# Performance work log

Measured on AMD Instinct MI355X. Metric: run time of the kernel, lower is better.

Reference implementation:

```python
import jax, jax.numpy as jnp
import numpy as np

B, CIN, H, W = 16, 1024, 32, 32
WIDTH = 256          # bottleneck width = planes * base_width/64 * cardinality
OUT = 1024           # planes * expansion
HEADS = WIDTH // 8   # 32
KS = 3               # kernel_size of SelfAttLayer


def unfold3x3(x):
    # x: (B, C, H, W) -> (B, C, 9, H, W), torch.nn.Unfold(3, padding=1) ordering (row-major kernel)
    xp = jnp.pad(x, ((0, 0), (0, 0), (1, 1), (1, 1)))
    h, w = x.shape[2], x.shape[3]
    patches = [xp[:, :, i:i + h, j:j + w] for i in range(KS) for j in range(KS)]
    return jnp.stack(patches, axis=2)


def bn(x, s, b):
    # inference-mode BatchNorm2d with running stats folded into per-channel scale/bias
    return x * s[None, :, None, None] + b[None, :, None, None]


def conv1x1(x, w):
    # w: (Cout, Cin)
    return jnp.einsum('bchw,oc->bohw', x, w)


def setup_inputs() -> dict:
    key = jax.random.key(0)
    ks = jax.random.split(key, 16)
    f = lambda k, shp, scale: (jax.random.normal(k, shp, dtype=jnp.float32) * scale)
    inp = {
        'x': f(ks[0], (B, CIN, H, W), 1.0),
        'w_conv1': f(ks[1], (WIDTH, CIN), 1.0 / np.sqrt(CIN)),
        'bn1_s': jnp.ones((WIDTH,), jnp.float32), 'bn1_b': jnp.zeros((WIDTH,), jnp.float32),
        'wq': f(ks[2], (WIDTH, WIDTH), 1.0 / np.sqrt(WIDTH)),
        'bnq_s': jnp.ones((WIDTH,), jnp.float32), 'bnq_b': jnp.zeros((WIDTH,), jnp.float32),
        'wk': f(ks[3], (WIDTH, WIDTH), 1.0 / np.sqrt(WIDTH)),
        'bnk_s': jnp.ones((WIDTH,), jnp.float32), 'bnk_b': jnp.zeros((WIDTH,), jnp.float32),
        'wv': f(ks[4], (WIDTH, WIDTH), 1.0 / np.sqrt(WIDTH)),
        'bnv_s': jnp.ones((WIDTH,), jnp.float32), 'bnv_b': jnp.zeros((WIDTH,), jnp.float32),
        'pos_h': f(ks[5], (WIDTH, KS, 1), 1.0),
        'pos_w': f(ks[6], (WIDTH, 1, KS), 1.0),
        'bnatt_s': jnp.ones((WIDTH,), jnp.float32), 'bnatt_b': jnp.zeros((WIDTH,), jnp.float32),
        'w_conv3': f(ks[7], (OUT, WIDTH), 1.0 / np.sqrt(WIDTH)),
        'bn3_s': jnp.ones((OUT,), jnp.float32), 'bn3_b': jnp.zeros((OUT,), jnp.float32),
    }
    return inp


def self_att(x, wq, bnq_s, bnq_b, wk, bnk_s, bnk_b, wv, bnv_s, bnv_b,
             pos_h, pos_w, bnatt_s, bnatt_b):
    b, c, h, w = x.shape
    d = c // HEADS
    q = jax.nn.relu(bn(conv1x1(x, wq), bnq_s, bnq_b))          # (B,C,H,W)
    k = jax.nn.relu(bn(conv1x1(x, wk), bnk_s, bnk_b))          # key_ks=1 -> 1x1 conv
    v = bn(conv1x1(x, wv), bnv_s, bnv_b)
    unfold_k = unfold3x3(k)                                     # (B,C,9,H,W)
    pos = (pos_h + pos_w).reshape(1, c, KS * KS, 1, 1)          # (1,C,9,1,1)
    kp = (unfold_k + pos).reshape(b, HEADS, d, KS * KS, h, w)
    qh = q.reshape(b, HEADS, d, h, w)
    attn = jnp.einsum('bgdhw,bgdkhw->bgkhw', qh, kp)            # (B,heads,9,H,W)
    attn = jax.nn.softmax(attn, axis=2)
    # local conv: each channel-group of size d shares its head's attention weights
    v_unf = unfold3x3(v).reshape(b, HEADS, d, KS * KS, h, w)
    out = jnp.einsum('bgdkhw,bgkhw->bgdhw', v_unf, attn).reshape(b, c, h, w)
    return jax.nn.relu(bn(out, bnatt_s, bnatt_b))


def reference(x, w_conv1, bn1_s, bn1_b, wq, bnq_s, bnq_b, wk, bnk_s, bnk_b,
              wv, bnv_s, bnv_b, pos_h, pos_w, bnatt_s, bnatt_b,
              w_conv3, bn3_s, bn3_b):
    residual = x
    h = jax.nn.relu(bn(conv1x1(x, w_conv1), bn1_s, bn1_b))
    h = self_att(h, wq, bnq_s, bnq_b, wk, bnk_s, bnk_b, wv, bnv_s, bnv_b,
                 pos_h, pos_w, bnatt_s, bnatt_b)
    h = bn(conv1x1(h, w_conv3), bn3_s, bn3_b)
    return jax.nn.relu(h + residual)
```

## Files before the change

### kernel.cpp

```cpp
#include <hip/hip_runtime.h>
#include <stdint.h>


typedef __attribute__((ext_vector_type(4))) float f32x4;
typedef __attribute__((ext_vector_type(8))) __bf16 bf16x8;
typedef __attribute__((ext_vector_type(4))) unsigned short u16x4;
typedef __attribute__((ext_vector_type(8))) unsigned short u16x8;

__device__ __forceinline__ float bf2f(unsigned short u) {
  union { unsigned int i; float f; } c; c.i = ((unsigned int)u) << 16; return c.f;
}
__device__ __forceinline__ unsigned short f2bf(float f) {
  union { float f; unsigned int i; } c; c.f = f;
  unsigned int x = c.i;
  return (unsigned short)((x + 0x7FFFu + ((x >> 16) & 1u)) >> 16);
}
__device__ __forceinline__ void gload_lds16(const unsigned short* g, unsigned short* l) {
  __builtin_amdgcn_global_load_lds(
      (const __attribute__((address_space(1))) unsigned int*)(const void*)g,
      (__attribute__((address_space(3))) unsigned int*)(void*)l, 16, 0, 0);
}

__global__ __launch_bounds__(256) void k_prep(
    const float* __restrict__ x, unsigned short* __restrict__ xt,
    const float* __restrict__ w1, const float* __restrict__ wq,
    const float* __restrict__ wk, const float* __restrict__ wv,
    const float* __restrict__ w3,
    const float* __restrict__ sq, const float* __restrict__ sk,
    const float* __restrict__ sv, const float* __restrict__ bq,
    const float* __restrict__ bk, const float* __restrict__ bv,
    unsigned short* __restrict__ w1b, unsigned short* __restrict__ wqkvb,
    unsigned short* __restrict__ w3b, float* __restrict__ sqkv,
    float* __restrict__ bqkv) {
  const int bid = blockIdx.x;
  if (bid < 16384) {
    __shared__ float tile[32][33];
    const int p0 = (bid & 31) * 32;
    const int c0 = ((bid >> 5) & 31) * 32;
    const int b  = bid >> 10;
    const int tx = threadIdx.x & 31;
    const int ty = threadIdx.x >> 5;
    const float* xb = x + (size_t)b * 1048576;
    unsigned short* xtb = xt + (size_t)b * 1048576;
#pragma unroll
    for (int i = 0; i < 4; ++i)
      tile[ty + i * 8][tx] = xb[(size_t)(c0 + ty + i * 8) * 1024 + p0 + tx];
    __syncthreads();
#pragma unroll
    for (int i = 0; i < 4; ++i)
      xtb[(size_t)(p0 + ty + i * 8) * 1024 + c0 + tx] = f2bf(tile[tx][ty + i * 8]);
    return;
  }
  const int idx = (bid - 16384) * 256 + threadIdx.x;
  if (idx < 262144) { w1b[idx] = f2bf(w1[idx]); return; }
  if (idx < 327680) { wqkvb[idx - 262144] = f2bf(wq[idx - 262144]); return; }
  if (idx < 393216) { wqkvb[idx - 262144] = f2bf(wk[idx - 327680]); return; }
  if (idx < 458752) { wqkvb[idx - 262144] = f2bf(wv[idx - 393216]); return; }
  if (idx < 720896) { w3b[idx - 458752] = f2bf(w3[idx - 458752]); return; }
  if (idx < 721664) {
    const int i = idx - 720896;
    sqkv[i] = i < 256 ? sq[i] : (i < 512 ? sk[i - 256] : sv[i - 512]);
    return;
  }
  if (idx < 722432) {
    const int i = idx - 721664;
    bqkv[i] = i < 256 ? bq[i] : (i < 512 ? bk[i - 256] : bv[i - 512]);
  }
}

template <int MF, int NF, int MODE>
__global__ __launch_bounds__(256, 3) void k_gemm_bt(
    const unsigned short* __restrict__ A, const unsigned short* __restrict__ B,
    void* __restrict__ CoutV, const float* __restrict__ scale,
    const float* __restrict__ bias, const unsigned short* __restrict__ resid_bf,
    int K, int relu_mask) {
  constexpr int BM = MF * 32, BN = NF * 32;
  __shared__ unsigned short lA[2][BM * 32];
  __shared__ unsigned short lB[2][BN * 32];
  const int m0 = blockIdx.y * BM;
  const int n0 = blockIdx.x * BN;
  const int tid = threadIdx.x;
  const int lane = tid & 63, wid = tid >> 6;
  const int wm = (wid >> 1) * (MF * 16), wn = (wid & 1) * (NF * 16);
  const int fr = lane & 15, fq = lane >> 4;
  const int cgr = (fq ^ (fr & 3)) * 8;

  f32x4 acc[MF][NF] = {};

  const int sr  = lane >> 2;
  const int scg = ((lane & 3) ^ (sr & 3)) * 8;
  const int warA = wid * (MF * 8);
  const int warB = wid * (NF * 8);
  const unsigned short* Asrc = A + (size_t)(m0 + warA + sr) * K + scg;
  const unsigned short* Bsrc = B + (size_t)(n0 + warB + sr) * K + scg;

  float rres[MF][NF][4];
  if (MODE == 1) {
#pragma unroll
    for (int i = 0; i < MF; ++i) {
      const int og = m0 + wm + i * 16 + fq * 4;
#pragma unroll
      for (int j = 0; j < NF; ++j) {
        const int P = n0 + wn + j * 16 + fr;
        const u16x4 rv = *(const u16x4*)&resid_bf[(size_t)P * 1024 + og];
#pragma unroll
        for (int rr = 0; rr < 4; ++rr) rres[i][j][rr] = bf2f(rv[rr]);
      }
    }
  }

#pragma unroll
  for (int u = 0; u < MF / 2; ++u)
    gload_lds16(Asrc + (size_t)u * 16 * K, &lA[0][(warA + u * 16) * 32]);
#pragma unroll
  for (int u = 0; u < NF / 2; ++u)
    gload_lds16(Bsrc + (size_t)u * 16 * K, &lB[0][(warB + u * 16) * 32]);
  __syncthreads();

  int p = 0;
  for (int k0 = 0; k0 < K; k0 += 32) {
    if (k0 + 32 < K) {
#pragma unroll
      for (int u = 0; u < MF / 2; ++u)
        gload_lds16(Asrc + (size_t)u * 16 * K + k0 + 32, &lA[p ^ 1][(warA + u * 16) * 32]);
#pragma unroll
      for (int u = 0; u < NF / 2; ++u)
        gload_lds16(Bsrc + (size_t)u * 16 * K + k0 + 32, &lB[p ^ 1][(warB + u * 16) * 32]);
    }

    bf16x8 af[MF], bb[NF];
#pragma unroll
    for (int i = 0; i < MF; ++i)
      af[i] = *(const bf16x8*)&lA[p][(wm + i * 16 + fr) * 32 + cgr];
#pragma unroll
    for (int j = 0; j < NF; ++j)
      bb[j] = *(const bf16x8*)&lB[p][(wn + j * 16 + fr) * 32 + cgr];
#pragma unroll
    for (int i = 0; i < MF; ++i)
#pragma unroll
      for (int j = 0; j < NF; ++j)
        acc[i][j] = __builtin_amdgcn_mfma_f32_16x16x32_bf16(af[i], bb[j], acc[i][j], 0, 0, 0);

    __syncthreads();
    p ^= 1;
  }

#pragma unroll
  for (int i = 0; i < MF; ++i) {
    const int og = m0 + wm + i * 16 + fq * 4;
    const f32x4 s4 = *(const f32x4*)&scale[og];
    const f32x4 b4 = *(const f32x4*)&bias[og];
#pragma unroll
    for (int j = 0; j < NF; ++j) {
      const int P = n0 + wn + j * 16 + fr;
      if (MODE == 0) {
        unsigned short* Cout = (unsigned short*)CoutV;
        const int do_relu = (relu_mask >> (og >> 8)) & 1;
        const size_t obase = (size_t)(og >> 8) * 4194304 + (size_t)P * 256 + (og & 255);
        u16x4 pk;
#pragma unroll
        for (int rr = 0; rr < 4; ++rr) {
          float v = acc[i][j][rr] * s4[rr] + b4[rr];
          if (do_relu) v = fmaxf(v, 0.0f);
          pk[rr] = f2bf(v);
        }
        *(u16x4*)&Cout[obase] = pk;
      } else {
        float* Cout = (float*)CoutV;
        const size_t base = (size_t)(P >> 10) * 1048576 + (size_t)(P & 1023);
#pragma unroll
        for (int rr = 0; rr < 4; ++rr) {
          float v = acc[i][j][rr] * s4[rr] + b4[rr] + rres[i][j][rr];
          Cout[base + (size_t)(og + rr) * 1024] = fmaxf(v, 0.0f);
        }
      }
    }
  }
}

__global__ __launch_bounds__(256, 4) void k_attn(
    const unsigned short* __restrict__ Q, const unsigned short* __restrict__ Kb,
    const unsigned short* __restrict__ Vb, unsigned short* __restrict__ O,
    const float* __restrict__ pos_h, const float* __restrict__ pos_w,
    const float* __restrict__ bs, const float* __restrict__ bb) {
  __shared__ float ph_l[3][256];
  __shared__ float pw_l[3][256];
  {
    const int c = threadIdx.x;
#pragma unroll
    for (int i = 0; i < 3; ++i) {
      ph_l[i][c] = pos_h[c * 3 + i];
      pw_l[i][c] = pos_w[c * 3 + i];
    }
  }
  __syncthreads();
  const int tid = threadIdx.x;
  const int g = tid & 31, s = tid >> 5;
  const int P = blockIdx.x * 8 + s;
  const int b = P >> 10, pix = P & 1023;
  const int hh = pix >> 5, ww = pix & 31;
  const int c0 = g * 8;

  float qf[8];
  {
    u16x8 qv = *(const u16x8*)&Q[(size_t)P * 256 + c0];
#pragma unroll
    for (int d = 0; d < 8; ++d) qf[d] = bf2f(qv[d]);
  }
  float Ai[3], Bj[3];
#pragma unroll
  for (int i = 0; i < 3; ++i) {
    float a = 0.f, w = 0.f;
#pragma unroll
    for (int d = 0; d < 8; ++d) {
      a += qf[d] * ph_l[i][c0 + d];
      w += qf[d] * pw_l[i][c0 + d];
    }
    Ai[i] = a; Bj[i] = w;
  }

  float S[9];
  int nPs[9];
#pragma unroll
  for (int t = 0; t < 9; ++t) {
    const int di = t / 3, dj = t % 3;
    const int nh = hh + di - 1, nw = ww + dj - 1;
    float sum = Ai[di] + Bj[dj];
    int nP = -1;
    if ((unsigned)nh < 32u && (unsigned)nw < 32u) {
      nP = (b << 10) + (nh << 5) + nw;
      u16x8 kv = *(const u16x8*)&Kb[(size_t)nP * 256 + c0];
#pragma unroll
      for (int d = 0; d < 8; ++d) sum += qf[d] * bf2f(kv[d]);
    }
    nPs[t] = nP;
    S[t] = sum;
  }

  float mx = S[0];
#pragma unroll
  for (int t = 1; t < 9; ++t) mx = fmaxf(mx, S[t]);
  float e[9], tot = 0.f;
#pragma unroll
  for (int t = 0; t < 9; ++t) { e[t] = __expf(S[t] - mx); tot += e[t]; }
  const float inv = 1.0f / tot;

  float of[8] = {0.f, 0.f, 0.f, 0.f, 0.f, 0.f, 0.f, 0.f};
#pragma unroll
  for (int t = 0; t < 9; ++t) {
    if (nPs[t] >= 0) {
      u16x8 vv = *(const u16x8*)&Vb[(size_t)nPs[t] * 256 + c0];
      const float w = e[t] * inv;
#pragma unroll
      for (int d = 0; d < 8; ++d) of[d] += w * bf2f(vv[d]);
    }
  }

  u16x8 res;
#pragma unroll
  for (int d = 0; d < 8; ++d) {
    float v = of[d] * bs[c0 + d] + bb[c0 + d];
    v = fmaxf(v, 0.0f);
    res[d] = f2bf(v);
  }
  *(u16x8*)&O[(size_t)P * 256 + c0] = res;
}

extern "C" void kernel_launch(void* const* d_in, const int* in_sizes, int n_in,
                              void* d_out, int out_size, void* d_ws, size_t ws_size,
                              hipStream_t stream) {
  (void)in_sizes; (void)n_in; (void)out_size; (void)ws_size;
  const float* x       = (const float*)d_in[0];
  const float* w1      = (const float*)d_in[1];
  const float* bn1_s   = (const float*)d_in[2];
  const float* bn1_b   = (const float*)d_in[3];
  const float* wq      = (const float*)d_in[4];
  const float* bnq_s   = (const float*)d_in[5];
  const float* bnq_b   = (const float*)d_in[6];
  const float* wk      = (const float*)d_in[7];
  const float* bnk_s   = (const float*)d_in[8];
  const float* bnk_b   = (const float*)d_in[9];
  const float* wv      = (const float*)d_in[10];
  const float* bnv_s   = (const float*)d_in[11];
  const float* bnv_b   = (const float*)d_in[12];
  const float* pos_h   = (const float*)d_in[13];
  const float* pos_w   = (const float*)d_in[14];
  const float* bnatt_s = (const float*)d_in[15];
  const float* bnatt_b = (const float*)d_in[16];
  const float* w3      = (const float*)d_in[17];
  const float* bn3_s   = (const float*)d_in[18];
  const float* bn3_b   = (const float*)d_in[19];

  char* ws = (char*)d_ws;
  unsigned short* h1t   = (unsigned short*)(ws);
  unsigned short* qkvt  = (unsigned short*)(ws + 8388608);
  unsigned short* att   = (unsigned short*)(ws + 33554432);
  unsigned short* xt    = (unsigned short*)(ws + 41943040);
  unsigned short* w1b   = (unsigned short*)(ws + 75497472);
  unsigned short* wqkvb = (unsigned short*)(ws + 76021760);
  unsigned short* w3b   = (unsigned short*)(ws + 76414976);
  float*          sqkv  = (float*)(ws + 76939264);
  float*          bqkv  = (float*)(ws + 76942336);

  k_prep<<<dim3(19206), dim3(256), 0, stream>>>(
      x, xt, w1, wq, wk, wv, w3, bnq_s, bnk_s, bnv_s, bnq_b, bnk_b, bnv_b,
      w1b, wqkvb, w3b, sqkv, bqkv);

  k_gemm_bt<2, 4, 0><<<dim3(128, 4), dim3(256), 0, stream>>>(
      w1b, xt, h1t, bn1_s, bn1_b, nullptr, 1024, 1);

  k_gemm_bt<4, 4, 0><<<dim3(128, 6), dim3(256), 0, stream>>>(
      wqkvb, h1t, qkvt, sqkv, bqkv, nullptr, 256, 3);

  k_attn<<<dim3(2048), dim3(256), 0, stream>>>(
      qkvt, qkvt + 4194304, qkvt + 8388608, att, pos_h, pos_w, bnatt_s, bnatt_b);

  k_gemm_bt<4, 2, 1><<<dim3(256, 8), dim3(256), 0, stream>>>(
      w3b, att, d_out, bn3_s, bn3_b, xt, 256, 0);
}
```

Baseline: 103.6 us.

## Swizzle GEMM block order across XCDs, retile GEMMs, defer residual load

Flattens the GEMM grid to 1D and remaps block IDs so that consecutive blocks assigned to the same XCD (bid&7) work on neighbouring tiles. The goal is better L2 reuse of the shared A/B tiles. The tile shapes change as well: conv1 goes to 128x64 tiles and conv3 to 128x128. The residual load in the final GEMM moves from before the K loop to after it and stays packed as bf16, which lowers register pressure during the MFMA loop. The trade-off is that the residual load latency is now exposed in the epilogue.

```diff
diff --git a/kernel.cpp b/kernel.cpp
--- a/kernel.cpp
+++ b/kernel.cpp
@@ -73,12 +73,16 @@
     const unsigned short* __restrict__ A, const unsigned short* __restrict__ B,
     void* __restrict__ CoutV, const float* __restrict__ scale,
     const float* __restrict__ bias, const unsigned short* __restrict__ resid_bf,
-    int K, int relu_mask) {
+    int K, int relu_mask, int gy) {
   constexpr int BM = MF * 32, BN = NF * 32;
   __shared__ unsigned short lA[2][BM * 32];
   __shared__ unsigned short lB[2][BN * 32];
-  const int m0 = blockIdx.y * BM;
-  const int n0 = blockIdx.x * BN;
+  const int nwg = gridDim.x;
+  const int bid = blockIdx.x;
+  const int swz = (bid & 7) * (nwg >> 3) + (bid >> 3);
+  const int bx = swz / gy, by = swz - bx * gy;
+  const int m0 = by * BM;
+  const int n0 = bx * BN;
   const int tid = threadIdx.x;
   const int lane = tid & 63, wid = tid >> 6;
   const int wm = (wid >> 1) * (MF * 16), wn = (wid & 1) * (NF * 16);
@@ -94,21 +98,6 @@
   const unsigned short* Asrc = A + (size_t)(m0 + warA + sr) * K + scg;
   const unsigned short* Bsrc = B + (size_t)(n0 + warB + sr) * K + scg;
 
-  float rres[MF][NF][4];
-  if (MODE == 1) {
-#pragma unroll
-    for (int i = 0; i < MF; ++i) {
-      const int og = m0 + wm + i * 16 + fq * 4;
-#pragma unroll
-      for (int j = 0; j < NF; ++j) {
-        const int P = n0 + wn + j * 16 + fr;
-        const u16x4 rv = *(const u16x4*)&resid_bf[(size_t)P * 1024 + og];
-#pragma unroll
-        for (int rr = 0; rr < 4; ++rr) rres[i][j][rr] = bf2f(rv[rr]);
-      }
-    }
-  }
-
 #pragma unroll
   for (int u = 0; u < MF / 2; ++u)
     gload_lds16(Asrc + (size_t)u * 16 * K, &lA[0][(warA + u * 16) * 32]);
@@ -143,6 +132,19 @@
 
     __syncthreads();
     p ^= 1;
+  }
+
+  u16x4 rp[MF][NF];
+  if (MODE == 1) {
+#pragma unroll
+    for (int i = 0; i < MF; ++i) {
+      const int og = m0 + wm + i * 16 + fq * 4;
+#pragma unroll
+      for (int j = 0; j < NF; ++j) {
+        const int P = n0 + wn + j * 16 + fr;
+        rp[i][j] = *(const u16x4*)&resid_bf[(size_t)P * 1024 + og];
+      }
+    }
   }
 
 #pragma unroll
@@ -170,7 +172,7 @@
         const size_t base = (size_t)(P >> 10) * 1048576 + (size_t)(P & 1023);
 #pragma unroll
         for (int rr = 0; rr < 4; ++rr) {
-          float v = acc[i][j][rr] * s4[rr] + b4[rr] + rres[i][j][rr];
+          float v = acc[i][j][rr] * s4[rr] + b4[rr] + bf2f(rp[i][j][rr]);
           Cout[base + (size_t)(og + rr) * 1024] = fmaxf(v, 0.0f);
         }
       }
@@ -306,15 +308,15 @@
       x, xt, w1, wq, wk, wv, w3, bnq_s, bnk_s, bnv_s, bnq_b, bnk_b, bnv_b,
       w1b, wqkvb, w3b, sqkv, bqkv);
 
-  k_gemm_bt<2, 4, 0><<<dim3(128, 4), dim3(256), 0, stream>>>(
-      w1b, xt, h1t, bn1_s, bn1_b, nullptr, 1024, 1);
-
-  k_gemm_bt<4, 4, 0><<<dim3(128, 6), dim3(256), 0, stream>>>(
-      wqkvb, h1t, qkvt, sqkv, bqkv, nullptr, 256, 3);
+  k_gemm_bt<4, 2, 0><<<dim3(512), dim3(256), 0, stream>>>(
+      w1b, xt, h1t, bn1_s, bn1_b, nullptr, 1024, 1, 2);
+
+  k_gemm_bt<4, 4, 0><<<dim3(768), dim3(256), 0, stream>>>(
+      wqkvb, h1t, qkvt, sqkv, bqkv, nullptr, 256, 3, 6);
 
   k_attn<<<dim3(2048), dim3(256), 0, stream>>>(
       qkvt, qkvt + 4194304, qkvt + 8388608, att, pos_h, pos_w, bnatt_s, bnatt_b);
 
-  k_gemm_bt<4, 2, 1><<<dim3(256, 8), dim3(256), 0, stream>>>(
-      w3b, att, d_out, bn3_s, bn3_b, xt, 256, 0);
-}
+  k_gemm_bt<4, 4, 1><<<dim3(1024), dim3(256), 0, stream>>>(
+      w3b, att, d_out, bn3_s, bn3_b, xt, 256, 0, 8);
+}
```

Result: no change. 102.6 us (-1.0%).
